# Kernel tuning notes

Measured on AMD Instinct MI355X. Metric: run time of the kernel, lower is better.

The kernel has to match this reference:

```python
import jax, jax.numpy as jnp
import numpy as np

DIM = 192
HEADS = 6
HIDDEN = 384  # int(DIM * 2.0)


def _ln(x, w, b):
    # WithBias LayerNorm over channel dim (torch normalizes last dim of b,(hw),c)
    mu = jnp.mean(x, axis=1, keepdims=True)
    var = jnp.var(x, axis=1, keepdims=True)
    return (x - mu) / jnp.sqrt(var + 1e-5) * w[None, :, None, None] + b[None, :, None, None]


def _conv1x1(x, w):  # w: [O, I, 1, 1]
    return jnp.einsum('bihw,oi->bohw', x, w[:, :, 0, 0])


def _dwconv3(x, w):  # depthwise 3x3, w: [C, 1, 3, 3]
    return jax.lax.conv_general_dilated(
        x, w, window_strides=(1, 1), padding=((1, 1), (1, 1)),
        feature_group_count=x.shape[1],
        dimension_numbers=('NCHW', 'OIHW', 'NCHW'))


def _l2norm(x):  # F.normalize along last axis
    n = jnp.sqrt(jnp.sum(x * x, axis=-1, keepdims=True))
    return x / jnp.maximum(n, 1e-12)


def setup_inputs() -> dict:
    key = jax.random.key(0)
    ks = jax.random.split(key, 16)
    s = 0.02
    d = {}
    d['x'] = jax.random.normal(ks[0], (2, DIM, 128, 128), dtype=jnp.float32)
    d['k_v'] = jax.random.normal(ks[1], (2, 256), dtype=jnp.float32)
    d['ln1_w'] = jnp.ones((DIM,), jnp.float32)
    d['ln1_b'] = jnp.zeros((DIM,), jnp.float32)
    d['temp'] = jnp.ones((HEADS, 1, 1), jnp.float32)
    d['w_kR'] = jax.random.normal(ks[2], (DIM * 3 // 4, 192), jnp.float32) * s
    d['w_kI'] = jax.random.normal(ks[3], (DIM // 4, 64), jnp.float32) * s
    d['w_qR'] = jax.random.normal(ks[4], (DIM, DIM * 3 // 4, 1, 1), jnp.float32) * s
    d['w_qdw'] = jax.random.normal(ks[5], (DIM, 1, 3, 3), jnp.float32) * s
    d['w_kvI'] = jax.random.normal(ks[6], (DIM * 2, DIM // 4, 1, 1), jnp.float32) * s
    d['w_kvdw'] = jax.random.normal(ks[7], (DIM * 2, 1, 3, 3), jnp.float32) * s
    d['w_po'] = jax.random.normal(ks[8], (DIM, DIM, 1, 1), jnp.float32) * s
    d['ln2_w'] = jnp.ones((DIM,), jnp.float32)
    d['ln2_b'] = jnp.zeros((DIM,), jnp.float32)
    d['w_ffk'] = jax.random.normal(ks[9], (DIM, 256), jnp.float32) * s
    d['w_pin'] = jax.random.normal(ks[10], (HIDDEN * 2, DIM, 1, 1), jnp.float32) * s
    d['w_dw'] = jax.random.normal(ks[11], (HIDDEN * 2, 1, 3, 3), jnp.float32) * s
    d['w_pout'] = jax.random.normal(ks[12], (DIM, HIDDEN, 1, 1), jnp.float32) * s
    return d


def reference(x, k_v, ln1_w, ln1_b, temp, w_kR, w_kI, w_qR, w_qdw, w_kvI, w_kvdw,
              w_po, ln2_w, ln2_b, w_ffk, w_pin, w_dw, w_pout):
    b, c, h, w = x.shape
    c3 = c * 3 // 4
    # ---- Rttention on norm1(x) ----
    xn = _ln(x, ln1_w, ln1_b)
    kvr = (k_v[:, :192] @ w_kR.T)[:, :, None, None]   # [b, 3c/4, 1, 1]
    kvi = (k_v[:, 192:] @ w_kI.T)[:, :, None, None]   # [b, c/4, 1, 1]
    x_r = xn[:, :c3] * kvr + xn[:, :c3]
    x_i = xn[:, c3:] * kvi + xn[:, c3:]
    q = _dwconv3(_conv1x1(x_r, w_qR), w_qdw)          # [b, c, h, w]
    kv = _dwconv3(_conv1x1(x_i, w_kvI), w_kvdw)       # [b, 2c, h, w]
    k, v = jnp.split(kv, 2, axis=1)
    rh = lambda t: t.reshape(b, HEADS, c // HEADS, h * w)
    q = _l2norm(rh(q))
    k = _l2norm(rh(k))
    v = rh(v)
    # channel-wise attention: [b, head, c_h, c_h]
    attn = jax.nn.softmax(jnp.einsum('bhcd,bhed->bhce', q, k) * temp[None], axis=-1)
    out = jnp.einsum('bhce,bhed->bhcd', attn, v).reshape(b, c, h, w)
    x = x + _conv1x1(out, w_po)
    # ---- GDFN FeedForward on norm2(x) ----
    xn2 = _ln(x, ln2_w, ln2_b)
    kvf = (k_v @ w_ffk.T)[:, :, None, None]           # [b, c, 1, 1]
    y = xn2 * kvf + xn2
    y = _dwconv3(_conv1x1(y, w_pin), w_dw)            # [b, 2*hidden, h, w]
    y1, y2 = jnp.split(y, 2, axis=1)
    y = jax.nn.gelu(y1, approximate=False) * y2
    x = x + _conv1x1(y, w_pout)
    return (x, k_v)
```

## Files before the change

kernel.cpp:

```cpp
#include <hip/hip_runtime.h>
#include <math.h>

#define HW 16384
#define IMG 128
#define CDIM 192
#define C3 144
#define C4 48
#define NB 2
#define NPX 32768
#define HEADS 6

typedef unsigned short u16;
typedef unsigned int u32;
typedef __attribute__((ext_vector_type(8))) short bf16x8;
typedef __attribute__((ext_vector_type(4))) float f32x4;

__device__ __forceinline__ float bf2f(u16 u) {
    return __uint_as_float(((unsigned int)u) << 16);
}
__device__ __forceinline__ u16 f2bf(float f) {
    unsigned int x = __float_as_uint(f);
    unsigned int r = x + 0x7fffu + ((x >> 16) & 1u);
    return (u16)(r >> 16);
}

static inline float* wsf(void* ws, size_t off) { return (float*)((char*)ws + off); }
static inline u16* wsh(void* ws, size_t off) { return (u16*)((char*)ws + off); }

__global__ void k_gemv(const float* __restrict__ kvv, const float* __restrict__ wkR,
                       const float* __restrict__ wkI, const float* __restrict__ wffk,
                       float* __restrict__ sm) {
    int t = blockIdx.x * 256 + threadIdx.x;
    if (t < 288) {
        int b = t / 144, o = t % 144;
        const float* v = kvv + b * 256;
        const float* w = wkR + o * 192;
        float s = 0.f;
        for (int j = 0; j < 192; j++) s += v[j] * w[j];
        sm[t] = s + 1.0f;
    } else if (t < 384) {
        int r = t - 288;
        int b = r / 48, o = r % 48;
        const float* v = kvv + b * 256 + 192;
        const float* w = wkI + o * 64;
        float s = 0.f;
        for (int j = 0; j < 64; j++) s += v[j] * w[j];
        sm[288 + r] = s + 1.0f;
    } else if (t < 768) {
        int r = t - 384;
        int b = r / 192, o = r % 192;
        const float* v = kvv + b * 256;
        const float* w = wffk + o * 256;
        float s = 0.f;
        for (int j = 0; j < 256; j++) s += v[j] * w[j];
        sm[384 + r] = s + 1.0f;
    }
}

__global__ void k_wconv(const float* __restrict__ wqR, const float* __restrict__ wkvI,
                        const float* __restrict__ wpo, const float* __restrict__ wpin,
                        const float* __restrict__ wpout, u16* __restrict__ wb) {
    int t = blockIdx.x * 256 + threadIdx.x;
    float v;
    if (t < 30720) {
        int o = t / 160, i = t % 160;
        v = (i < 144) ? wqR[o * 144 + i] : 0.f;
    } else if (t < 55296) {
        int r = t - 30720; int o = r / 64, i = r % 64;
        v = (i < 48) ? wkvI[o * 48 + i] : 0.f;
    } else if (t < 92160) {
        v = wpo[t - 55296];
    } else if (t < 239616) {
        v = wpin[t - 92160];
    } else {
        v = wpout[t - 239616];
    }
    wb[t] = f2bf(v);
}

__global__ __launch_bounds__(256) void k_ln_mod(
    const float* __restrict__ x, const float* __restrict__ lnw, const float* __restrict__ lnb,
    const float* __restrict__ sca, const float* __restrict__ scb,
    u16* __restrict__ outA, u16* __restrict__ outB) {
    int g = blockIdx.x * 256 + threadIdx.x;
    int b = g >> 14, p = g & 16383;
    const float* xp = x + (size_t)b * CDIM * HW + p;
    float s = 0.f, s2 = 0.f;
    for (int c = 0; c < CDIM; c++) { float v = xp[(size_t)c * HW]; s += v; s2 += v * v; }
    float mu = s * (1.0f / CDIM);
    float var = s2 * (1.0f / CDIM) - mu * mu;
    float rstd = rsqrtf(var + 1e-5f);
    if (outB) {
        for (int c = 0; c < C3; c++) {
            float v = xp[(size_t)c * HW];
            float xn = (v - mu) * rstd * lnw[c] + lnb[c];
            outA[((size_t)b * C3 + c) * HW + p] = f2bf(xn * sca[b * C3 + c]);
        }
        for (int c = 0; c < C4; c++) {
            float v = xp[(size_t)(C3 + c) * HW];
            float xn = (v - mu) * rstd * lnw[C3 + c] + lnb[C3 + c];
            outB[((size_t)b * C4 + c) * HW + p] = f2bf(xn * scb[b * C4 + c]);
        }
    } else {
        for (int c = 0; c < CDIM; c++) {
            float v = xp[(size_t)c * HW];
            float xn = (v - mu) * rstd * lnw[c] + lnb[c];
            outA[((size_t)b * CDIM + c) * HW + p] = f2bf(xn * sca[b * CDIM + c]);
        }
    }
}

template <int NCH, bool RESID>
__global__ __launch_bounds__(256) void k_gemm(
    const u16* __restrict__ X, int xrows,
    const u16* __restrict__ Wb,
    const float* __restrict__ resid,
    u16* __restrict__ outb, float* __restrict__ outf, int CO) {
    constexpr int CIP = NCH * 32;
    __shared__ __align__(16) u16 Ws[64 * 32];
    __shared__ __align__(16) u16 Xs[32 * 130];
    const int tid = threadIdx.x;
    const int n0 = blockIdx.x * 128;
    const int m0 = blockIdx.y * 64;
    const int b = blockIdx.z;
    const u16* Xb = X + (size_t)b * xrows * HW + n0;
    const int wave = tid >> 6, lane = tid & 63;
    const int quad = lane >> 4, l16 = lane & 15;
    const int smr = tid >> 2, sk4 = tid & 3;
    const int skr = tid >> 3, sc0 = (tid & 7) * 16;
    f32x4 acc[4][2] = {};
    for (int ch = 0; ch < NCH; ch++) {
        const int k0 = ch * 32;
        if (ch) __syncthreads();
        {
            const int4 wv = *(const int4*)(Wb + (size_t)(m0 + smr) * CIP + k0 + sk4 * 8);
            *(int4*)&Ws[(smr << 5) + (((sk4 ^ (smr & 3)) & 3) << 3)] = wv;
        }
        {
            const u16* xc = Xb + (size_t)(k0 + skr) * HW + sc0;
            int4 r0 = *(const int4*)xc;
            int4 r1 = *(const int4*)(xc + 8);
            u32* dst = (u32*)&Xs[skr * 130 + sc0];
#pragma unroll
            for (int i = 0; i < 4; i++) dst[i] = ((const u32*)&r0)[i];
#pragma unroll
            for (int i = 0; i < 4; i++) dst[4 + i] = ((const u32*)&r1)[i];
        }
        __syncthreads();
        bf16x8 af[4];
#pragma unroll
        for (int mi = 0; mi < 4; mi++) {
            int row = mi * 16 + l16;
            af[mi] = *(const bf16x8*)&Ws[(row << 5) + ((quad ^ (row & 3)) << 3)];
        }
#pragma unroll
        for (int ni = 0; ni < 2; ni++) {
            int n = wave * 32 + ni * 16 + l16;
            bf16x8 bfr;
#pragma unroll
            for (int j = 0; j < 8; j++) bfr[j] = (short)Xs[(quad * 8 + j) * 130 + n];
#pragma unroll
            for (int mi = 0; mi < 4; mi++)
                acc[mi][ni] = __builtin_amdgcn_mfma_f32_16x16x32_bf16(af[mi], bfr, acc[mi][ni], 0, 0, 0);
        }
    }
#pragma unroll
    for (int mi = 0; mi < 4; mi++) {
#pragma unroll
        for (int ni = 0; ni < 2; ni++) {
#pragma unroll
            for (int r = 0; r < 4; r++) {
                int m = m0 + mi * 16 + quad * 4 + r;
                int n = n0 + wave * 32 + ni * 16 + l16;
                size_t idx = ((size_t)b * CO + m) * HW + n;
                float v = acc[mi][ni][r];
                if (RESID) outf[idx] = v + resid[idx];
                else outb[idx] = f2bf(v);
            }
        }
    }
}

__global__ __launch_bounds__(256) void k_dw2(const u16* __restrict__ X,
                                             const float* __restrict__ Wd,
                                             u16* __restrict__ out, int C, int sqCh,
                                             float* __restrict__ sqacc) {
    __shared__ float In[34 * 132];
    __shared__ float red[4];
    int bc = blockIdx.x >> 2, rt = blockIdx.x & 3;
    int b = bc / C, ch = bc % C;
    const u16* xb = X + (size_t)bc * HW;
    int t = threadIdx.x;
    int c0 = (t & 7) * 16;
    for (int r = t >> 3; r < 34; r += 32) {
        int y = rt * 32 - 1 + r;
        float* dst = &In[r * 132 + 1 + c0];
        if ((unsigned)y < 128u) {
            const u16* src = xb + y * 128 + c0;
            int4 r0 = *(const int4*)src;
            int4 r1 = *(const int4*)(src + 8);
            const u16* p0 = (const u16*)&r0;
            const u16* p1 = (const u16*)&r1;
#pragma unroll
            for (int i = 0; i < 8; i++) dst[i] = bf2f(p0[i]);
#pragma unroll
            for (int i = 0; i < 8; i++) dst[8 + i] = bf2f(p1[i]);
        } else {
#pragma unroll
            for (int i = 0; i < 16; i++) dst[i] = 0.f;
        }
    }
    if (t < 34) { In[t * 132] = 0.f; In[t * 132 + 129] = 0.f; }
    __syncthreads();
    const float* w = Wd + ch * 9;
    float w00 = w[0], w01 = w[1], w02 = w[2], w10 = w[3], w11 = w[4],
          w12 = w[5], w20 = w[6], w21 = w[7], w22 = w[8];
    int x = t & 127, rg = t >> 7;
    int base = rg * 16;
    float A2 = 0.f, A1 = 0.f, B1 = 0.f, ssq = 0.f;
    u16* ob = out + (size_t)bc * HW + (rt * 32 + base) * 128 + x;
#pragma unroll
    for (int r = 0; r < 18; r++) {
        const float* row = &In[(base + r) * 132 + x];
        float v0 = row[0], v1 = row[1], v2 = row[2];
        float h0 = w00 * v0 + w01 * v1 + w02 * v2;
        float h1 = w10 * v0 + w11 * v1 + w12 * v2;
        float h2 = w20 * v0 + w21 * v1 + w22 * v2;
        if (r >= 2) {
            float val = A2 + B1 + h2;
            ob[(size_t)(r - 2) * 128] = f2bf(val);
            ssq += val * val;
        }
        A2 = A1; A1 = h0; B1 = h1;
    }
    if (ch < sqCh) {
        for (int o = 32; o > 0; o >>= 1) ssq += __shfl_down(ssq, o, 64);
        int wid = t >> 6, lane = t & 63;
        if (lane == 0) red[wid] = ssq;
        __syncthreads();
        if (t == 0) atomicAdd(&sqacc[b * 192 + ch], red[0] + red[1] + red[2] + red[3]);
    }
}

__global__ __launch_bounds__(256) void k_dw_gelu2(const u16* __restrict__ G0,
                                                  const float* __restrict__ Wd,
                                                  u16* __restrict__ out) {
    __shared__ float In[2 * 34 * 132];
    int bc = blockIdx.x >> 2, rt = blockIdx.x & 3;
    int b = bc / 384, j = bc % 384;
    int t = threadIdx.x;
    int c0 = (t & 7) * 16;
    for (int pl = 0; pl < 2; pl++) {
        const u16* xb = G0 + ((size_t)b * 768 + pl * 384 + j) * HW;
        float* pla = &In[pl * 34 * 132];
        for (int r = t >> 3; r < 34; r += 32) {
            int y = rt * 32 - 1 + r;
            float* dst = &pla[r * 132 + 1 + c0];
            if ((unsigned)y < 128u) {
                const u16* src = xb + y * 128 + c0;
                int4 r0 = *(const int4*)src;
                int4 r1 = *(const int4*)(src + 8);
                const u16* p0 = (const u16*)&r0;
                const u16* p1 = (const u16*)&r1;
#pragma unroll
                for (int i = 0; i < 8; i++) dst[i] = bf2f(p0[i]);
#pragma unroll
                for (int i = 0; i < 8; i++) dst[8 + i] = bf2f(p1[i]);
            } else {
#pragma unroll
                for (int i = 0; i < 16; i++) dst[i] = 0.f;
            }
        }
        if (t < 34) { pla[t * 132] = 0.f; pla[t * 132 + 129] = 0.f; }
    }
    __syncthreads();
    const float* w1 = Wd + j * 9;
    const float* w2 = Wd + (384 + j) * 9;
    float a00 = w1[0], a01 = w1[1], a02 = w1[2], a10 = w1[3], a11 = w1[4],
          a12 = w1[5], a20 = w1[6], a21 = w1[7], a22 = w1[8];
    float b00 = w2[0], b01 = w2[1], b02 = w2[2], b10 = w2[3], b11 = w2[4],
          b12 = w2[5], b20 = w2[6], b21 = w2[7], b22 = w2[8];
    int x = t & 127, rg = t >> 7;
    int base = rg * 16;
    float A2a = 0.f, A1a = 0.f, B1a = 0.f;
    float A2b = 0.f, A1b = 0.f, B1b = 0.f;
    u16* ob = out + ((size_t)b * 384 + j) * HW + (rt * 32 + base) * 128 + x;
#pragma unroll
    for (int r = 0; r < 18; r++) {
        const float* r1p = &In[(base + r) * 132 + x];
        const float* r2p = r1p + 34 * 132;
        float u0 = r1p[0], u1 = r1p[1], u2 = r1p[2];
        float v0 = r2p[0], v1 = r2p[1], v2 = r2p[2];
        float h0a = a00 * u0 + a01 * u1 + a02 * u2;
        float h1a = a10 * u0 + a11 * u1 + a12 * u2;
        float h2a = a20 * u0 + a21 * u1 + a22 * u2;
        float h0b = b00 * v0 + b01 * v1 + b02 * v2;
        float h1b = b10 * v0 + b11 * v1 + b12 * v2;
        float h2b = b20 * v0 + b21 * v1 + b22 * v2;
        if (r >= 2) {
            float s1 = A2a + B1a + h2a;
            float s2 = A2b + B1b + h2b;
            float g = 0.5f * s1 * (1.0f + erff(s1 * 0.70710678118654752f));
            ob[(size_t)(r - 2) * 128] = f2bf(g * s2);
        }
        A2a = A1a; A1a = h0a; B1a = h1a;
        A2b = A1b; A1b = h0b; B1b = h1b;
    }
}

__global__ __launch_bounds__(256) void k_qk(const u16* __restrict__ qb_,
                                            const u16* __restrict__ kb_,
                                            float* __restrict__ S) {
    int bx = blockIdx.x;
    int bh = bx >> 6, ds = bx & 63;
    int b = bh / HEADS, h = bh % HEADS;
    int tid = threadIdx.x;
    int wave = tid >> 6, lane = tid & 63;
    int quad = lane >> 4, l16 = lane & 15;
    int tm = wave >> 1, tn = wave & 1;
    const u16* qrow = qb_ + ((size_t)(b * 192 + h * 32 + tm * 16 + l16)) * HW + ds * 256 + quad * 8;
    const u16* krow = kb_ + ((size_t)(b * 384 + h * 32 + tn * 16 + l16)) * HW + ds * 256 + quad * 8;
    f32x4 acc = {};
#pragma unroll
    for (int ch = 0; ch < 8; ch++) {
        bf16x8 a = *(const bf16x8*)(qrow + ch * 32);
        bf16x8 k8 = *(const bf16x8*)(krow + ch * 32);
        acc = __builtin_amdgcn_mfma_f32_16x16x32_bf16(a, k8, acc, 0, 0, 0);
    }
    float* Sb = S + bh * 1024;
#pragma unroll
    for (int r = 0; r < 4; r++)
        atomicAdd(&Sb[(tm * 16 + quad * 4 + r) * 32 + tn * 16 + l16], acc[r]);
}

__global__ void k_softmax(const float* __restrict__ S, const float* __restrict__ sqq,
                          const float* __restrict__ sqk, const float* __restrict__ temp,
                          u16* __restrict__ attnb) {
    int row = blockIdx.x;
    int bh = row >> 5, c2 = row & 31;
    int b = bh / HEADS, h = bh % HEADS;
    int e = threadIdx.x;
    float l = -1e30f;
    if (e < 32) {
        float invq = 1.0f / fmaxf(sqrtf(sqq[b * 192 + h * 32 + c2]), 1e-12f);
        float invk = 1.0f / fmaxf(sqrtf(sqk[b * 192 + h * 32 + e]), 1e-12f);
        l = S[bh * 1024 + c2 * 32 + e] * invq * invk * temp[h];
    }
    float m = l;
    for (int o = 32; o > 0; o >>= 1) m = fmaxf(m, __shfl_xor(m, o, 64));
    float ev = (e < 32) ? expf(l - m) : 0.f;
    float ssum = ev;
    for (int o = 32; o > 0; o >>= 1) ssum += __shfl_xor(ssum, o, 64);
    if (e < 32) attnb[bh * 1024 + c2 * 32 + e] = f2bf(ev / ssum);
}

__global__ __launch_bounds__(256) void k_av(const u16* __restrict__ attnb,
                                            const u16* __restrict__ kvb,
                                            u16* __restrict__ out) {
    __shared__ __align__(16) u16 Vs[32 * 130];
    int bh = blockIdx.x >> 7;
    int pt = blockIdx.x & 127;
    int b = bh / HEADS, h = bh % HEADS;
    int p0 = pt * 128;
    int t = threadIdx.x;
    {
        int e = t >> 3, c0 = (t & 7) * 16;
        const u16* src = kvb + ((size_t)(b * 384 + 192 + h * 32 + e)) * HW + p0 + c0;
        int4 r0 = *(const int4*)src;
        int4 r1 = *(const int4*)(src + 8);
        u32* dst = (u32*)&Vs[e * 130 + c0];
#pragma unroll
        for (int i = 0; i < 4; i++) dst[i] = ((const u32*)&r0)[i];
#pragma unroll
        for (int i = 0; i < 4; i++) dst[4 + i] = ((const u32*)&r1)[i];
    }
    __syncthreads();
    int wave = t >> 6, lane = t & 63;
    int quad = lane >> 4, l16 = lane & 15;
    f32x4 acc[2][2] = {};
    bf16x8 af[2];
#pragma unroll
    for (int tm = 0; tm < 2; tm++)
        af[tm] = *(const bf16x8*)(attnb + bh * 1024 + (tm * 16 + l16) * 32 + quad * 8);
#pragma unroll
    for (int nt = 0; nt < 2; nt++) {
        int n = wave * 32 + nt * 16 + l16;
        bf16x8 bfr;
#pragma unroll
        for (int j = 0; j < 8; j++) bfr[j] = (short)Vs[(quad * 8 + j) * 130 + n];
#pragma unroll
        for (int tm = 0; tm < 2; tm++)
            acc[tm][nt] = __builtin_amdgcn_mfma_f32_16x16x32_bf16(af[tm], bfr, acc[tm][nt], 0, 0, 0);
    }
#pragma unroll
    for (int tm = 0; tm < 2; tm++)
#pragma unroll
        for (int nt = 0; nt < 2; nt++)
#pragma unroll
            for (int r = 0; r < 4; r++) {
                int c = h * 32 + tm * 16 + quad * 4 + r;
                int p = p0 + wave * 32 + nt * 16 + l16;
                out[((size_t)b * 192 + c) * HW + p] = f2bf(acc[tm][nt][r]);
            }
}

__global__ void k_copy(const float* __restrict__ kvv, float* __restrict__ out) {
    int t = blockIdx.x * 256 + threadIdx.x;
    if (t < 512) out[t] = kvv[t];
}

extern "C" void kernel_launch(void* const* d_in, const int* in_sizes, int n_in,
                              void* d_out, int out_size, void* d_ws, size_t ws_size,
                              hipStream_t stream) {
    const float* x     = (const float*)d_in[0];
    const float* k_v   = (const float*)d_in[1];
    const float* ln1w  = (const float*)d_in[2];
    const float* ln1b  = (const float*)d_in[3];
    const float* temp  = (const float*)d_in[4];
    const float* w_kR  = (const float*)d_in[5];
    const float* w_kI  = (const float*)d_in[6];
    const float* w_qR  = (const float*)d_in[7];
    const float* w_qdw = (const float*)d_in[8];
    const float* w_kvI = (const float*)d_in[9];
    const float* w_kvdw= (const float*)d_in[10];
    const float* w_po  = (const float*)d_in[11];
    const float* ln2w  = (const float*)d_in[12];
    const float* ln2b  = (const float*)d_in[13];
    const float* w_ffk = (const float*)d_in[14];
    const float* w_pin = (const float*)d_in[15];
    const float* w_dw  = (const float*)d_in[16];
    const float* w_pout= (const float*)d_in[17];
    float* out = (float*)d_out;

    const size_t MiB = 1048576ULL;
    u16*   q0b     = wsh(d_ws, 0);
    u16*   attnoutb= wsh(d_ws, 0);
    u16*   y0b     = wsh(d_ws, 0);
    u16*   kv0b    = wsh(d_ws, 12 * MiB);
    u16*   ybufb   = wsh(d_ws, 12 * MiB);
    float* x1      = wsf(d_ws, 36 * MiB);
    u16*   qbuf_b  = wsh(d_ws, 84 * MiB);
    u16*   kvbuf_b = wsh(d_ws, 96 * MiB);
    u16*   xrb     = wsh(d_ws, 120 * MiB);
    u16*   xib     = wsh(d_ws, 130 * MiB);
    u16*   g0b     = wsh(d_ws, 134 * MiB);
    u16*   wb      = wsh(d_ws, 182 * MiB);
    float* sm      = wsf(d_ws, 183 * MiB);
    u16* wq   = wb;
    u16* wkv  = wb + 30720;
    u16* wpo  = wb + 55296;
    u16* wpin = wb + 92160;
    u16* wpout= wb + 239616;
    float* kvr  = sm;
    float* kvi  = sm + 288;
    float* kvf  = sm + 384;
    float* sqq  = sm + 768;
    float* sqk  = sm + 1152;
    float* Smat = sm + 1536;
    u16*   attnb= (u16*)(sm + 13824);

    hipMemsetAsync(sm + 768, 0, (768 + 12288) * sizeof(float), stream);

    k_wconv<<<1224, 256, 0, stream>>>(w_qR, w_kvI, w_po, w_pin, w_pout, wb);
    k_gemv<<<3, 256, 0, stream>>>(k_v, w_kR, w_kI, w_ffk, sm);
    k_ln_mod<<<NPX / 256, 256, 0, stream>>>(x, ln1w, ln1b, kvr, kvi, xrb, xib);
    k_gemm<5, false><<<dim3(128, 3, 2), 256, 0, stream>>>(xrb, 144, wq, nullptr, q0b, nullptr, 192);
    k_gemm<2, false><<<dim3(128, 6, 2), 256, 0, stream>>>(xib, 48, wkv, nullptr, kv0b, nullptr, 384);
    k_dw2<<<NB * 192 * 4, 256, 0, stream>>>(q0b, w_qdw, qbuf_b, 192, 192, sqq);
    k_dw2<<<NB * 384 * 4, 256, 0, stream>>>(kv0b, w_kvdw, kvbuf_b, 384, 192, sqk);
    k_qk<<<12 * 64, 256, 0, stream>>>(qbuf_b, kvbuf_b, Smat);
    k_softmax<<<384, 64, 0, stream>>>(Smat, sqq, sqk, temp, attnb);
    k_av<<<12 * 128, 256, 0, stream>>>(attnb, kvbuf_b, attnoutb);
    k_gemm<6, true><<<dim3(128, 3, 2), 256, 0, stream>>>(attnoutb, 192, wpo, x, nullptr, x1, 192);
    k_ln_mod<<<NPX / 256, 256, 0, stream>>>(x1, ln2w, ln2b, kvf, nullptr, y0b, nullptr);
    k_gemm<6, false><<<dim3(128, 12, 2), 256, 0, stream>>>(y0b, 192, wpin, nullptr, g0b, nullptr, 768);
    k_dw_gelu2<<<NB * 384 * 4, 256, 0, stream>>>(g0b, w_dw, ybufb);
    k_gemm<12, true><<<dim3(128, 3, 2), 256, 0, stream>>>(ybufb, 384, wpout, x1, nullptr, out, 192);
    k_copy<<<2, 256, 0, stream>>>(k_v, out + (size_t)NB * CDIM * HW);
}
```

Before: 300.9 us.

## Rework LayerNorm, store residual in bf16, drop atomics and merge setup kernels

The LayerNorm kernel is rewritten so each block handles 64 pixels with vectorized loads, splits the channel reduction across 16 thread groups via shared memory, and keeps values in registers instead of reading x twice. The intermediate residual x1 is now stored as bf16 instead of fp32, which halves its write and read traffic but adds rounding error to the residual path. Atomic accumulation in the QK and sum-of-squares kernels is replaced by per-tile partial buffers that the softmax sums, which removes the memset and atomics. Weight conversion, the GEMVs and the k_v copy are merged into one setup kernel to cut launch count.

```diff
diff --git a/kernel.cpp b/kernel.cpp
--- a/kernel.cpp
+++ b/kernel.cpp
@@ -27,95 +27,139 @@
 static inline float* wsf(void* ws, size_t off) { return (float*)((char*)ws + off); }
 static inline u16* wsh(void* ws, size_t off) { return (u16*)((char*)ws + off); }
 
-__global__ void k_gemv(const float* __restrict__ kvv, const float* __restrict__ wkR,
-                       const float* __restrict__ wkI, const float* __restrict__ wffk,
-                       float* __restrict__ sm) {
+__global__ void k_setup(const float* __restrict__ kvv, const float* __restrict__ wkR,
+                        const float* __restrict__ wkI, const float* __restrict__ wffk,
+                        const float* __restrict__ wqR, const float* __restrict__ wkvI,
+                        const float* __restrict__ wpo, const float* __restrict__ wpin,
+                        const float* __restrict__ wpout,
+                        u16* __restrict__ wb, float* __restrict__ sm,
+                        float* __restrict__ tail) {
     int t = blockIdx.x * 256 + threadIdx.x;
-    if (t < 288) {
-        int b = t / 144, o = t % 144;
-        const float* v = kvv + b * 256;
-        const float* w = wkR + o * 192;
-        float s = 0.f;
-        for (int j = 0; j < 192; j++) s += v[j] * w[j];
-        sm[t] = s + 1.0f;
-    } else if (t < 384) {
-        int r = t - 288;
-        int b = r / 48, o = r % 48;
-        const float* v = kvv + b * 256 + 192;
-        const float* w = wkI + o * 64;
-        float s = 0.f;
-        for (int j = 0; j < 64; j++) s += v[j] * w[j];
-        sm[288 + r] = s + 1.0f;
-    } else if (t < 768) {
-        int r = t - 384;
-        int b = r / 192, o = r % 192;
-        const float* v = kvv + b * 256;
-        const float* w = wffk + o * 256;
-        float s = 0.f;
-        for (int j = 0; j < 256; j++) s += v[j] * w[j];
-        sm[384 + r] = s + 1.0f;
-    }
-}
-
-__global__ void k_wconv(const float* __restrict__ wqR, const float* __restrict__ wkvI,
-                        const float* __restrict__ wpo, const float* __restrict__ wpin,
-                        const float* __restrict__ wpout, u16* __restrict__ wb) {
-    int t = blockIdx.x * 256 + threadIdx.x;
-    float v;
-    if (t < 30720) {
-        int o = t / 160, i = t % 160;
-        v = (i < 144) ? wqR[o * 144 + i] : 0.f;
-    } else if (t < 55296) {
-        int r = t - 30720; int o = r / 64, i = r % 64;
-        v = (i < 48) ? wkvI[o * 48 + i] : 0.f;
-    } else if (t < 92160) {
-        v = wpo[t - 55296];
-    } else if (t < 239616) {
-        v = wpin[t - 92160];
-    } else {
-        v = wpout[t - 239616];
-    }
-    wb[t] = f2bf(v);
-}
-
-__global__ __launch_bounds__(256) void k_ln_mod(
-    const float* __restrict__ x, const float* __restrict__ lnw, const float* __restrict__ lnb,
+    if (t < 313344) {
+        float v;
+        if (t < 30720) {
+            int o = t / 160, i = t % 160;
+            v = (i < 144) ? wqR[o * 144 + i] : 0.f;
+        } else if (t < 55296) {
+            int r = t - 30720; int o = r / 64, i = r % 64;
+            v = (i < 48) ? wkvI[o * 48 + i] : 0.f;
+        } else if (t < 92160) {
+            v = wpo[t - 55296];
+        } else if (t < 239616) {
+            v = wpin[t - 92160];
+        } else {
+            v = wpout[t - 239616];
+        }
+        wb[t] = f2bf(v);
+    } else if (t < 314112) {
+        int r = t - 313344;
+        if (r < 288) {
+            int b = r / 144, o = r % 144;
+            const float* v = kvv + b * 256;
+            const float* w = wkR + o * 192;
+            float s = 0.f;
+            for (int j = 0; j < 192; j++) s += v[j] * w[j];
+            sm[r] = s + 1.0f;
+        } else if (r < 384) {
+            int r2 = r - 288;
+            int b = r2 / 48, o = r2 % 48;
+            const float* v = kvv + b * 256 + 192;
+            const float* w = wkI + o * 64;
+            float s = 0.f;
+            for (int j = 0; j < 64; j++) s += v[j] * w[j];
+            sm[288 + r2] = s + 1.0f;
+        } else {
+            int r2 = r - 384;
+            int b = r2 / 192, o = r2 % 192;
+            const float* v = kvv + b * 256;
+            const float* w = wffk + o * 256;
+            float s = 0.f;
+            for (int j = 0; j < 256; j++) s += v[j] * w[j];
+            sm[384 + r2] = s + 1.0f;
+        }
+    } else if (t < 314624) {
+        int r = t - 314112;
+        tail[r] = kvv[r];
+    }
+}
+
+template <bool INBF, bool SPLIT>
+__global__ __launch_bounds__(256) void k_ln(
+    const void* __restrict__ xin,
+    const float* __restrict__ lnw, const float* __restrict__ lnb,
     const float* __restrict__ sca, const float* __restrict__ scb,
     u16* __restrict__ outA, u16* __restrict__ outB) {
-    int g = blockIdx.x * 256 + threadIdx.x;
-    int b = g >> 14, p = g & 16383;
-    const float* xp = x + (size_t)b * CDIM * HW + p;
-    float s = 0.f, s2 = 0.f;
-    for (int c = 0; c < CDIM; c++) { float v = xp[(size_t)c * HW]; s += v; s2 += v * v; }
-    float mu = s * (1.0f / CDIM);
-    float var = s2 * (1.0f / CDIM) - mu * mu;
-    float rstd = rsqrtf(var + 1e-5f);
-    if (outB) {
-        for (int c = 0; c < C3; c++) {
-            float v = xp[(size_t)c * HW];
-            float xn = (v - mu) * rstd * lnw[c] + lnb[c];
-            outA[((size_t)b * C3 + c) * HW + p] = f2bf(xn * sca[b * C3 + c]);
-        }
-        for (int c = 0; c < C4; c++) {
-            float v = xp[(size_t)(C3 + c) * HW];
-            float xn = (v - mu) * rstd * lnw[C3 + c] + lnb[C3 + c];
-            outB[((size_t)b * C4 + c) * HW + p] = f2bf(xn * scb[b * C4 + c]);
-        }
-    } else {
-        for (int c = 0; c < CDIM; c++) {
-            float v = xp[(size_t)c * HW];
-            float xn = (v - mu) * rstd * lnw[c] + lnb[c];
-            outA[((size_t)b * CDIM + c) * HW + p] = f2bf(xn * sca[b * CDIM + c]);
-        }
-    }
-}
-
-template <int NCH, bool RESID>
+    __shared__ float red[2][16][16][4];
+    __shared__ float mu_s[16][4], rstd_s[16][4];
+    int t = threadIdx.x;
+    int px4 = t & 15, cg = t >> 4;
+    int base = blockIdx.x * 64;
+    int b = base >> 14;
+    int p = (base & 16383) + px4 * 4;
+    float vals[12][4];
+    float s[4] = {0.f, 0.f, 0.f, 0.f}, s2[4] = {0.f, 0.f, 0.f, 0.f};
+#pragma unroll
+    for (int j = 0; j < 12; j++) {
+        int c = cg * 12 + j;
+        size_t off = ((size_t)(b * CDIM + c)) * HW + p;
+        float v[4];
+        if (INBF) {
+            ushort4 u = *(const ushort4*)((const u16*)xin + off);
+            v[0] = bf2f(u.x); v[1] = bf2f(u.y); v[2] = bf2f(u.z); v[3] = bf2f(u.w);
+        } else {
+            float4 f = *(const float4*)((const float*)xin + off);
+            v[0] = f.x; v[1] = f.y; v[2] = f.z; v[3] = f.w;
+        }
+#pragma unroll
+        for (int q = 0; q < 4; q++) {
+            vals[j][q] = v[q]; s[q] += v[q]; s2[q] += v[q] * v[q];
+        }
+    }
+#pragma unroll
+    for (int q = 0; q < 4; q++) { red[0][cg][px4][q] = s[q]; red[1][cg][px4][q] = s2[q]; }
+    __syncthreads();
+    if (t < 16) {
+        float S[4] = {0.f, 0.f, 0.f, 0.f}, S2[4] = {0.f, 0.f, 0.f, 0.f};
+        for (int g2 = 0; g2 < 16; g2++)
+#pragma unroll
+            for (int q = 0; q < 4; q++) { S[q] += red[0][g2][t][q]; S2[q] += red[1][g2][t][q]; }
+#pragma unroll
+        for (int q = 0; q < 4; q++) {
+            float mu = S[q] * (1.0f / CDIM);
+            float var = S2[q] * (1.0f / CDIM) - mu * mu;
+            mu_s[t][q] = mu;
+            rstd_s[t][q] = rsqrtf(var + 1e-5f);
+        }
+    }
+    __syncthreads();
+    float mu[4], rs[4];
+#pragma unroll
+    for (int q = 0; q < 4; q++) { mu[q] = mu_s[px4][q]; rs[q] = rstd_s[px4][q]; }
+#pragma unroll
+    for (int j = 0; j < 12; j++) {
+        int c = cg * 12 + j;
+        float w = lnw[c], bb = lnb[c];
+        float sc; u16* op; size_t off;
+        if (SPLIT) {
+            if (c < C3) { sc = sca[b * C3 + c]; off = ((size_t)(b * C3 + c)) * HW + p; op = outA; }
+            else { sc = scb[b * C4 + c - C3]; off = ((size_t)(b * C4 + c - C3)) * HW + p; op = outB; }
+        } else {
+            sc = sca[b * CDIM + c]; off = ((size_t)(b * CDIM + c)) * HW + p; op = outA;
+        }
+        ushort4 o;
+        o.x = f2bf(((vals[j][0] - mu[0]) * rs[0] * w + bb) * sc);
+        o.y = f2bf(((vals[j][1] - mu[1]) * rs[1] * w + bb) * sc);
+        o.z = f2bf(((vals[j][2] - mu[2]) * rs[2] * w + bb) * sc);
+        o.w = f2bf(((vals[j][3] - mu[3]) * rs[3] * w + bb) * sc);
+        *(ushort4*)(op + off) = o;
+    }
+}
+
+template <int NCH, int MODE>
 __global__ __launch_bounds__(256) void k_gemm(
     const u16* __restrict__ X, int xrows,
     const u16* __restrict__ Wb,
-    const float* __restrict__ resid,
-    u16* __restrict__ outb, float* __restrict__ outf, int CO) {
+    const void* __restrict__ resid, void* __restrict__ outp, int CO) {
     constexpr int CIP = NCH * 32;
     __shared__ __align__(16) u16 Ws[64 * 32];
     __shared__ __align__(16) u16 Xs[32 * 130];
@@ -174,8 +218,15 @@
                 int n = n0 + wave * 32 + ni * 16 + l16;
                 size_t idx = ((size_t)b * CO + m) * HW + n;
                 float v = acc[mi][ni][r];
-                if (RESID) outf[idx] = v + resid[idx];
-                else outb[idx] = f2bf(v);
+                if (MODE == 0) {
+                    ((u16*)outp)[idx] = f2bf(v);
+                } else if (MODE == 1) {
+                    v += ((const float*)resid)[idx];
+                    ((u16*)outp)[idx] = f2bf(v);
+                } else {
+                    v += bf2f(((const u16*)resid)[idx]);
+                    ((float*)outp)[idx] = v;
+                }
             }
         }
     }
@@ -184,7 +235,7 @@
 __global__ __launch_bounds__(256) void k_dw2(const u16* __restrict__ X,
                                              const float* __restrict__ Wd,
                                              u16* __restrict__ out, int C, int sqCh,
-                                             float* __restrict__ sqacc) {
+                                             float* __restrict__ sqp) {
     __shared__ float In[34 * 132];
     __shared__ float red[4];
     int bc = blockIdx.x >> 2, rt = blockIdx.x & 3;
@@ -238,7 +289,7 @@
         int wid = t >> 6, lane = t & 63;
         if (lane == 0) red[wid] = ssq;
         __syncthreads();
-        if (t == 0) atomicAdd(&sqacc[b * 192 + ch], red[0] + red[1] + red[2] + red[3]);
+        if (t == 0) sqp[((b * 192 + ch) << 2) | rt] = red[0] + red[1] + red[2] + red[3];
     }
 }
 
@@ -310,31 +361,30 @@
 
 __global__ __launch_bounds__(256) void k_qk(const u16* __restrict__ qb_,
                                             const u16* __restrict__ kb_,
-                                            float* __restrict__ S) {
-    int bx = blockIdx.x;
-    int bh = bx >> 6, ds = bx & 63;
+                                            float* __restrict__ Spart) {
+    int bh = blockIdx.x >> 5, ds = blockIdx.x & 31;
     int b = bh / HEADS, h = bh % HEADS;
     int tid = threadIdx.x;
     int wave = tid >> 6, lane = tid & 63;
     int quad = lane >> 4, l16 = lane & 15;
     int tm = wave >> 1, tn = wave & 1;
-    const u16* qrow = qb_ + ((size_t)(b * 192 + h * 32 + tm * 16 + l16)) * HW + ds * 256 + quad * 8;
-    const u16* krow = kb_ + ((size_t)(b * 384 + h * 32 + tn * 16 + l16)) * HW + ds * 256 + quad * 8;
+    const u16* qrow = qb_ + ((size_t)(b * 192 + h * 32 + tm * 16 + l16)) * HW + ds * 512 + quad * 8;
+    const u16* krow = kb_ + ((size_t)(b * 384 + h * 32 + tn * 16 + l16)) * HW + ds * 512 + quad * 8;
     f32x4 acc = {};
 #pragma unroll
-    for (int ch = 0; ch < 8; ch++) {
+    for (int ch = 0; ch < 16; ch++) {
         bf16x8 a = *(const bf16x8*)(qrow + ch * 32);
         bf16x8 k8 = *(const bf16x8*)(krow + ch * 32);
         acc = __builtin_amdgcn_mfma_f32_16x16x32_bf16(a, k8, acc, 0, 0, 0);
     }
-    float* Sb = S + bh * 1024;
+    float* Sb = Spart + ((size_t)ds * 12 + bh) * 1024;
 #pragma unroll
     for (int r = 0; r < 4; r++)
-        atomicAdd(&Sb[(tm * 16 + quad * 4 + r) * 32 + tn * 16 + l16], acc[r]);
-}
-
-__global__ void k_softmax(const float* __restrict__ S, const float* __restrict__ sqq,
-                          const float* __restrict__ sqk, const float* __restrict__ temp,
+        Sb[(tm * 16 + quad * 4 + r) * 32 + tn * 16 + l16] = acc[r];
+}
+
+__global__ void k_softmax(const float* __restrict__ Spart, const float* __restrict__ sqqp,
+                          const float* __restrict__ sqkp, const float* __restrict__ temp,
                           u16* __restrict__ attnb) {
     int row = blockIdx.x;
     int bh = row >> 5, c2 = row & 31;
@@ -342,9 +392,15 @@
     int e = threadIdx.x;
     float l = -1e30f;
     if (e < 32) {
-        float invq = 1.0f / fmaxf(sqrtf(sqq[b * 192 + h * 32 + c2]), 1e-12f);
-        float invk = 1.0f / fmaxf(sqrtf(sqk[b * 192 + h * 32 + e]), 1e-12f);
-        l = S[bh * 1024 + c2 * 32 + e] * invq * invk * temp[h];
+        float s = 0.f;
+        for (int d = 0; d < 32; d++) s += Spart[((size_t)d * 12 + bh) * 1024 + c2 * 32 + e];
+        const float* qp = sqqp + (b * 192 + h * 32 + c2) * 4;
+        const float* kp = sqkp + (b * 192 + h * 32 + e) * 4;
+        float nq = qp[0] + qp[1] + qp[2] + qp[3];
+        float nk = kp[0] + kp[1] + kp[2] + kp[3];
+        float invq = 1.0f / fmaxf(sqrtf(nq), 1e-12f);
+        float invk = 1.0f / fmaxf(sqrtf(nk), 1e-12f);
+        l = s * invq * invk * temp[h];
     }
     float m = l;
     for (int o = 32; o > 0; o >>= 1) m = fmaxf(m, __shfl_xor(m, o, 64));
@@ -402,11 +458,6 @@
                 int p = p0 + wave * 32 + nt * 16 + l16;
                 out[((size_t)b * 192 + c) * HW + p] = f2bf(acc[tm][nt][r]);
             }
-}
-
-__global__ void k_copy(const float* __restrict__ kvv, float* __restrict__ out) {
-    int t = blockIdx.x * 256 + threadIdx.x;
-    if (t < 512) out[t] = kvv[t];
 }
 
 extern "C" void kernel_launch(void* const* d_in, const int* in_sizes, int n_in,
@@ -438,14 +489,15 @@
     u16*   y0b     = wsh(d_ws, 0);
     u16*   kv0b    = wsh(d_ws, 12 * MiB);
     u16*   ybufb   = wsh(d_ws, 12 * MiB);
-    float* x1      = wsf(d_ws, 36 * MiB);
-    u16*   qbuf_b  = wsh(d_ws, 84 * MiB);
-    u16*   kvbuf_b = wsh(d_ws, 96 * MiB);
-    u16*   xrb     = wsh(d_ws, 120 * MiB);
-    u16*   xib     = wsh(d_ws, 130 * MiB);
-    u16*   g0b     = wsh(d_ws, 134 * MiB);
-    u16*   wb      = wsh(d_ws, 182 * MiB);
-    float* sm      = wsf(d_ws, 183 * MiB);
+    u16*   x1b     = wsh(d_ws, 36 * MiB);
+    u16*   qbuf_b  = wsh(d_ws, 48 * MiB);
+    u16*   kvbuf_b = wsh(d_ws, 60 * MiB);
+    u16*   xrb     = wsh(d_ws, 84 * MiB);
+    u16*   xib     = wsh(d_ws, 94 * MiB);
+    u16*   g0b     = wsh(d_ws, 98 * MiB);
+    u16*   wb      = wsh(d_ws, 146 * MiB);
+    float* sm      = wsf(d_ws, 147 * MiB);
+    float* Spart   = wsf(d_ws, 148 * MiB);
     u16* wq   = wb;
     u16* wkv  = wb + 30720;
     u16* wpo  = wb + 55296;
@@ -454,27 +506,24 @@
     float* kvr  = sm;
     float* kvi  = sm + 288;
     float* kvf  = sm + 384;
-    float* sqq  = sm + 768;
-    float* sqk  = sm + 1152;
-    float* Smat = sm + 1536;
-    u16*   attnb= (u16*)(sm + 13824);
-
-    hipMemsetAsync(sm + 768, 0, (768 + 12288) * sizeof(float), stream);
-
-    k_wconv<<<1224, 256, 0, stream>>>(w_qR, w_kvI, w_po, w_pin, w_pout, wb);
-    k_gemv<<<3, 256, 0, stream>>>(k_v, w_kR, w_kI, w_ffk, sm);
-    k_ln_mod<<<NPX / 256, 256, 0, stream>>>(x, ln1w, ln1b, kvr, kvi, xrb, xib);
-    k_gemm<5, false><<<dim3(128, 3, 2), 256, 0, stream>>>(xrb, 144, wq, nullptr, q0b, nullptr, 192);
-    k_gemm<2, false><<<dim3(128, 6, 2), 256, 0, stream>>>(xib, 48, wkv, nullptr, kv0b, nullptr, 384);
-    k_dw2<<<NB * 192 * 4, 256, 0, stream>>>(q0b, w_qdw, qbuf_b, 192, 192, sqq);
-    k_dw2<<<NB * 384 * 4, 256, 0, stream>>>(kv0b, w_kvdw, kvbuf_b, 384, 192, sqk);
-    k_qk<<<12 * 64, 256, 0, stream>>>(qbuf_b, kvbuf_b, Smat);
-    k_softmax<<<384, 64, 0, stream>>>(Smat, sqq, sqk, temp, attnb);
+    float* sqqp = sm + 768;
+    float* sqkp = sm + 2304;
+    u16*   attnb= (u16*)(sm + 3840);
+
+    k_setup<<<1229, 256, 0, stream>>>(k_v, w_kR, w_kI, w_ffk, w_qR, w_kvI, w_po,
+                                      w_pin, w_pout, wb, sm,
+                                      out + (size_t)NB * CDIM * HW);
+    k_ln<false, true><<<NPX / 64, 256, 0, stream>>>(x, ln1w, ln1b, kvr, kvi, xrb, xib);
+    k_gemm<5, 0><<<dim3(128, 3, 2), 256, 0, stream>>>(xrb, 144, wq, nullptr, q0b, 192);
+    k_gemm<2, 0><<<dim3(128, 6, 2), 256, 0, stream>>>(xib, 48, wkv, nullptr, kv0b, 384);
+    k_dw2<<<NB * 192 * 4, 256, 0, stream>>>(q0b, w_qdw, qbuf_b, 192, 192, sqqp);
+    k_dw2<<<NB * 384 * 4, 256, 0, stream>>>(kv0b, w_kvdw, kvbuf_b, 384, 192, sqkp);
+    k_qk<<<12 * 32, 256, 0, stream>>>(qbuf_b, kvbuf_b, Spart);
+    k_softmax<<<384, 64, 0, stream>>>(Spart, sqqp, sqkp, temp, attnb);
     k_av<<<12 * 128, 256, 0, stream>>>(attnb, kvbuf_b, attnoutb);
-    k_gemm<6, true><<<dim3(128, 3, 2), 256, 0, stream>>>(attnoutb, 192, wpo, x, nullptr, x1, 192);
-    k_ln_mod<<<NPX / 256, 256, 0, stream>>>(x1, ln2w, ln2b, kvf, nullptr, y0b, nullptr);
-    k_gemm<6, false><<<dim3(128, 12, 2), 256, 0, stream>>>(y0b, 192, wpin, nullptr, g0b, nullptr, 768);
+    k_gemm<6, 1><<<dim3(128, 3, 2), 256, 0, stream>>>(attnoutb, 192, wpo, x, x1b, 192);
+    k_ln<true, false><<<NPX / 64, 256, 0, stream>>>(x1b, ln2w, ln2b, kvf, nullptr, y0b, nullptr);
+    k_gemm<6, 0><<<dim3(128, 12, 2), 256, 0, stream>>>(y0b, 192, wpin, nullptr, g0b, 768);
     k_dw_gelu2<<<NB * 384 * 4, 256, 0, stream>>>(g0b, w_dw, ybufb);
-    k_gemm<12, true><<<dim3(128, 3, 2), 256, 0, stream>>>(ybufb, 384, wpout, x1, nullptr, out, 192);
-    k_copy<<<2, 256, 0, stream>>>(k_v, out + (size_t)NB * CDIM * HW);
-}
+    k_gemm<12, 2><<<dim3(128, 3, 2), 256, 0, stream>>>(ybufb, 384, wpout, x1b, out, 192);
+}
```

New measurement: 268.6 us. -10.8%, faster.
